# Performance work log

Measured on AMD Instinct MI355X. Metric: run time of the kernel, lower is better.

## Reference

```python
import jax, jax.numpy as jnp
import numpy as np

ALPHA = 0.01  # LeakyReLU negative slope


def setup_inputs() -> dict:
    key = jax.random.key(0)
    k1, k2, k3 = jax.random.split(key, 3)
    B, T, F, U, E = 32, 512, 128, 64, 32
    x = jax.random.normal(k1, (B, T, F), dtype=jnp.float32)
    Wg = jax.random.normal(k2, (F, E), dtype=jnp.float32) * (1.0 / np.sqrt(F))
    bg = jnp.zeros((E,), dtype=jnp.float32)
    We = jax.random.normal(k3, (E, F, U), dtype=jnp.float32) * (1.0 / np.sqrt(F))
    be = jnp.zeros((E, U), dtype=jnp.float32)
    return {"x": x, "Wg": Wg, "bg": bg, "We": We, "be": be}


def reference(x, Wg, bg, We, be):
    # gate: linear (no softmax in the original)
    gate = jnp.einsum('btf,fe->bte', x, Wg) + bg            # [B,T,E]
    # all experts as one batched GEMM: [B,T,U,E]
    h = jnp.einsum('btf,efu->btue', x, We) + be.T            # be.T: [U,E]
    h = jnp.where(h >= 0, h, ALPHA * h)                      # LeakyReLU
    # weighted sum over experts
    out = jnp.einsum('btue,bte->btu', h, gate)               # [B,T,U]
    return out
```

## Files before the change

### kernel.cpp

```cpp
#include <hip/hip_runtime.h>
#include <stdint.h>

#define N_TOK 16384
#define F_DIM 128
#define U_DIM 64
#define E_DIM 32

typedef __bf16 bf16x8 __attribute__((ext_vector_type(8)));
typedef float  floatx4 __attribute__((ext_vector_type(4)));

#define MFMA16(a, b, c) __builtin_amdgcn_mfma_f32_16x16x32_bf16((a), (b), (c), 0, 0, 0)

__device__ __forceinline__ unsigned short f2bf(float f) {
  union { float f; unsigned u; } v; v.f = f;
  unsigned r = v.u + 0x7FFFu + ((v.u >> 16) & 1u);
  return (unsigned short)(r >> 16);
}

__global__ __launch_bounds__(512, 1) void moe_main(
    const float* __restrict__ x,
    const float* __restrict__ Wg,
    const float* __restrict__ bg,
    const float* __restrict__ We,
    const float* __restrict__ be,
    float* __restrict__ out) {
  __shared__ unsigned short Xs[64 * 136];
  __shared__ float Gs[E_DIM][68];

  const int tid  = threadIdx.x;
  const int lane = tid & 63;
  const int wid  = tid >> 6;
  const int quad = lane >> 4;
  const int l15  = lane & 15;
  const int wr   = wid >> 2;
  const int wc   = wid & 3;
  const int u    = wc * 16 + l15;
  const int base = blockIdx.x * 64;

  float bw[4][4][8];
  float bevb[4];
  {
    const float* wsrc = We + (size_t)(quad * 8) * 64 + u;
#pragma unroll
    for (int e0 = 0; e0 < 3; e0++) {
#pragma unroll
      for (int ks = 0; ks < 4; ks++)
#pragma unroll
        for (int j = 0; j < 8; j++)
          bw[e0][ks][j] = wsrc[(size_t)e0 * 8192 + (ks * 32 + j) * 64];
      bevb[e0] = be[e0 * U_DIM + u];
    }
  }

  {
    const int row = tid >> 3;
    const int c16 = tid & 7;
    const float4* src = (const float4*)(x + (size_t)(base + row) * F_DIM + c16 * 16);
    float4 v0 = src[0], v1 = src[1], v2 = src[2], v3 = src[3];
    union { unsigned short us[16]; uint4 q[2]; } pk;
    pk.us[0]  = f2bf(v0.x); pk.us[1]  = f2bf(v0.y); pk.us[2]  = f2bf(v0.z); pk.us[3]  = f2bf(v0.w);
    pk.us[4]  = f2bf(v1.x); pk.us[5]  = f2bf(v1.y); pk.us[6]  = f2bf(v1.z); pk.us[7]  = f2bf(v1.w);
    pk.us[8]  = f2bf(v2.x); pk.us[9]  = f2bf(v2.y); pk.us[10] = f2bf(v2.z); pk.us[11] = f2bf(v2.w);
    pk.us[12] = f2bf(v3.x); pk.us[13] = f2bf(v3.y); pk.us[14] = f2bf(v3.z); pk.us[15] = f2bf(v3.w);
    uint4* dst = (uint4*)&Xs[row * 136 + c16 * 16];
    dst[0] = pk.q[0];
    dst[1] = pk.q[1];
  }
  __syncthreads();

  {
    const int rg = wid >> 1;
    const int et = wid & 1;
    bf16x8 ag[4];
#pragma unroll
    for (int ks = 0; ks < 4; ks++)
      ag[ks] = *(const bf16x8*)&Xs[(rg * 16 + l15) * 136 + ks * 32 + quad * 8];
    floatx4 g = {0.f, 0.f, 0.f, 0.f};
#pragma unroll
    for (int ks = 0; ks < 4; ks++) {
      union { unsigned short us[8]; bf16x8 v; } p;
#pragma unroll
      for (int j = 0; j < 8; j++)
        p.us[j] = f2bf(Wg[(size_t)(ks * 32 + quad * 8 + j) * 32 + et * 16 + l15]);
      g = MFMA16(ag[ks], p.v, g);
    }
    float bgv = bg[et * 16 + l15];
#pragma unroll
    for (int r = 0; r < 4; r++)
      Gs[et * 16 + l15][rg * 16 + quad * 4 + r] = g[r] + bgv;
  }

  bf16x8 a[2][4];
#pragma unroll
  for (int mb = 0; mb < 2; mb++)
#pragma unroll
    for (int ks = 0; ks < 4; ks++)
      a[mb][ks] = *(const bf16x8*)&Xs[(wr * 32 + mb * 16 + l15) * 136 + ks * 32 + quad * 8];
  __syncthreads();

  float oacc[8];
#pragma unroll
  for (int i = 0; i < 8; i++) oacc[i] = 0.f;

  float4 gbuf[2][2];
#pragma unroll
  for (int mb = 0; mb < 2; mb++)
    gbuf[0][mb] = *(const float4*)&Gs[0][wr * 32 + mb * 16 + quad * 4];

  const float* wbase = We + (size_t)(quad * 8) * 64 + u;

#pragma unroll 4
  for (int e = 0; e < E_DIM; ++e) {
    const int c = e & 3;
    const int gp = e & 1;

    if (e + 3 < E_DIM) {
#pragma unroll
      for (int ks = 0; ks < 4; ks++)
#pragma unroll
        for (int j = 0; j < 8; j++)
          bw[(e + 3) & 3][ks][j] = wbase[(size_t)(e + 3) * 8192 + (ks * 32 + j) * 64];
      bevb[(e + 3) & 3] = be[(e + 3) * U_DIM + u];
    }
    if (e + 1 < E_DIM) {
#pragma unroll
      for (int mb = 0; mb < 2; mb++)
        gbuf[gp ^ 1][mb] = *(const float4*)&Gs[e + 1][wr * 32 + mb * 16 + quad * 4];
    }

    bf16x8 bb[4];
#pragma unroll
    for (int ks = 0; ks < 4; ks++) {
      union { unsigned short us[8]; bf16x8 v; } p;
#pragma unroll
      for (int j = 0; j < 8; j++) p.us[j] = f2bf(bw[c][ks][j]);
      bb[ks] = p.v;
    }

    const float bev = bevb[c];
    floatx4 h[2];
#pragma unroll
    for (int mb = 0; mb < 2; mb++) h[mb] = {bev, bev, bev, bev};
#pragma unroll
    for (int ks = 0; ks < 4; ks++)
#pragma unroll
      for (int mb = 0; mb < 2; mb++)
        h[mb] = MFMA16(a[mb][ks], bb[ks], h[mb]);

#pragma unroll
    for (int mb = 0; mb < 2; mb++) {
      const float4 g4 = gbuf[gp][mb];
      const float gr[4] = {g4.x, g4.y, g4.z, g4.w};
#pragma unroll
      for (int r = 0; r < 4; r++) {
        float t = h[mb][r];
        t = fmaxf(t, 0.01f * t);
        oacc[mb * 4 + r] = fmaf(gr[r], t, oacc[mb * 4 + r]);
      }
    }
  }

#pragma unroll
  for (int mb = 0; mb < 2; mb++)
#pragma unroll
    for (int r = 0; r < 4; r++)
      out[(size_t)(base + wr * 32 + mb * 16 + quad * 4 + r) * U_DIM + u] = oacc[mb * 4 + r];
}

extern "C" void kernel_launch(void* const* d_in, const int* in_sizes, int n_in,
                              void* d_out, int out_size, void* d_ws, size_t ws_size,
                              hipStream_t stream) {
  const float* x  = (const float*)d_in[0];
  const float* Wg = (const float*)d_in[1];
  const float* bg = (const float*)d_in[2];
  const float* We = (const float*)d_in[3];
  const float* be = (const float*)d_in[4];
  (void)in_sizes; (void)n_in; (void)out_size; (void)d_ws; (void)ws_size;

  moe_main<<<N_TOK / 64, 512, 0, stream>>>(x, Wg, bg, We, be, (float*)d_out);
}
```

Baseline: 97.54 us.

## Stage expert weights cooperatively through double-buffered LDS as bf16

Previously every wave loaded its own fp32 copy of each expert's weight slice from global memory and converted it to bf16 itself, which is redundant because waves sharing columns load the same data. Now the 512 threads cooperatively load each expert's 128x64 weight matrix once per block, convert it to bf16, and store it into a double-buffered LDS array. The MFMA loop reads B fragments from LDS and waits on a barrier each expert iteration. This cuts global traffic and per-wave conversion work, but adds a barrier per expert and extra LDS use and traffic.

```diff
diff --git a/kernel.cpp b/kernel.cpp
--- a/kernel.cpp
+++ b/kernel.cpp
@@ -17,15 +17,23 @@
   return (unsigned short)(r >> 16);
 }
 
-__global__ __launch_bounds__(512, 1) void moe_main(
+__device__ __forceinline__ uint4 cvt8pack(const float* w) {
+  union { __bf16 b[8]; uint4 q; } p;
+#pragma unroll
+  for (int j = 0; j < 8; j++) p.b[j] = (__bf16)w[j];
+  return p.q;
+}
+
+__global__ __launch_bounds__(512, 1) void moe_fused(
     const float* __restrict__ x,
     const float* __restrict__ Wg,
     const float* __restrict__ bg,
     const float* __restrict__ We,
     const float* __restrict__ be,
     float* __restrict__ out) {
-  __shared__ unsigned short Xs[64 * 136];
-  __shared__ float Gs[E_DIM][68];
+  __shared__ __align__(16) unsigned short Xs[64 * 136];
+  __shared__ __align__(16) float Gs[E_DIM][68];
+  __shared__ __align__(16) unsigned short Bs[2][16 * 528];
 
   const int tid  = threadIdx.x;
   const int lane = tid & 63;
@@ -37,20 +45,14 @@
   const int u    = wc * 16 + l15;
   const int base = blockIdx.x * 64;
 
-  float bw[4][4][8];
-  float bevb[4];
-  {
-    const float* wsrc = We + (size_t)(quad * 8) * 64 + u;
+  const int f0 = (wid >> 2) * 32 + (wid & 3) * 8;
+  const float* ws0 = We + f0 * 64 + lane;
+
+  float w0[8], w1[8];
 #pragma unroll
-    for (int e0 = 0; e0 < 3; e0++) {
-#pragma unroll
-      for (int ks = 0; ks < 4; ks++)
-#pragma unroll
-        for (int j = 0; j < 8; j++)
-          bw[e0][ks][j] = wsrc[(size_t)e0 * 8192 + (ks * 32 + j) * 64];
-      bevb[e0] = be[e0 * U_DIM + u];
-    }
-  }
+  for (int j = 0; j < 8; j++) { w0[j] = ws0[j * 64]; w1[j] = ws0[4096 + j * 64]; }
+  float bevCur = be[u];
+  float bevNxt = be[U_DIM + u];
 
   {
     const int row = tid >> 3;
@@ -66,6 +68,11 @@
     dst[0] = pk.q[0];
     dst[1] = pk.q[1];
   }
+
+  *(uint4*)&Bs[0][wid * 528 + lane * 8]       = cvt8pack(w0);
+  *(uint4*)&Bs[0][(wid + 8) * 528 + lane * 8] = cvt8pack(w1);
+#pragma unroll
+  for (int j = 0; j < 8; j++) { w0[j] = ws0[8192 + j * 64]; w1[j] = ws0[8192 + 4096 + j * 64]; }
   __syncthreads();
 
   {
@@ -102,61 +109,56 @@
 #pragma unroll
   for (int i = 0; i < 8; i++) oacc[i] = 0.f;
 
-  float4 gbuf[2][2];
+  const unsigned short* rB = Bs[0];
+  unsigned short*       wB = Bs[1];
+
+  for (int e = 0; e < E_DIM; ++e) {
+    bf16x8 bb[4];
 #pragma unroll
-  for (int mb = 0; mb < 2; mb++)
-    gbuf[0][mb] = *(const float4*)&Gs[0][wr * 32 + mb * 16 + quad * 4];
+    for (int ks = 0; ks < 4; ks++)
+      bb[ks] = *(const bf16x8*)&rB[(ks * 4 + quad) * 528 + u * 8];
+    float4 gc0 = *(const float4*)&Gs[e][wr * 32 + quad * 4];
+    float4 gc1 = *(const float4*)&Gs[e][wr * 32 + 16 + quad * 4];
 
-  const float* wbase = We + (size_t)(quad * 8) * 64 + u;
+    if (e < E_DIM - 1) {
+      *(uint4*)&wB[wid * 528 + lane * 8]       = cvt8pack(w0);
+      *(uint4*)&wB[(wid + 8) * 528 + lane * 8] = cvt8pack(w1);
+      if (e < E_DIM - 2) {
+        const float* s = ws0 + (size_t)(e + 2) * 8192;
+#pragma unroll
+        for (int j = 0; j < 8; j++) { w0[j] = s[j * 64]; w1[j] = s[4096 + j * 64]; }
+      }
+    }
+    float bevNew = (e < E_DIM - 2) ? be[(e + 2) * U_DIM + u] : 0.f;
 
-#pragma unroll 4
-  for (int e = 0; e < E_DIM; ++e) {
-    const int c = e & 3;
-    const int gp = e & 1;
+    asm volatile("s_waitcnt lgkmcnt(0)" ::: "memory");
+    __builtin_amdgcn_sched_barrier(0);
 
-    if (e + 3 < E_DIM) {
+    floatx4 h0 = {bevCur, bevCur, bevCur, bevCur};
+    floatx4 h1 = h0;
 #pragma unroll
-      for (int ks = 0; ks < 4; ks++)
-#pragma unroll
-        for (int j = 0; j < 8; j++)
-          bw[(e + 3) & 3][ks][j] = wbase[(size_t)(e + 3) * 8192 + (ks * 32 + j) * 64];
-      bevb[(e + 3) & 3] = be[(e + 3) * U_DIM + u];
-    }
-    if (e + 1 < E_DIM) {
-#pragma unroll
-      for (int mb = 0; mb < 2; mb++)
-        gbuf[gp ^ 1][mb] = *(const float4*)&Gs[e + 1][wr * 32 + mb * 16 + quad * 4];
+    for (int ks = 0; ks < 4; ks++) {
+      h0 = MFMA16(a[0][ks], bb[ks], h0);
+      h1 = MFMA16(a[1][ks], bb[ks], h1);
     }
 
-    bf16x8 bb[4];
-#pragma unroll
-    for (int ks = 0; ks < 4; ks++) {
-      union { unsigned short us[8]; bf16x8 v; } p;
-#pragma unroll
-      for (int j = 0; j < 8; j++) p.us[j] = f2bf(bw[c][ks][j]);
-      bb[ks] = p.v;
-    }
-
-    const float bev = bevb[c];
-    floatx4 h[2];
-#pragma unroll
-    for (int mb = 0; mb < 2; mb++) h[mb] = {bev, bev, bev, bev};
-#pragma unroll
-    for (int ks = 0; ks < 4; ks++)
-#pragma unroll
-      for (int mb = 0; mb < 2; mb++)
-        h[mb] = MFMA16(a[mb][ks], bb[ks], h[mb]);
-
-#pragma unroll
-    for (int mb = 0; mb < 2; mb++) {
-      const float4 g4 = gbuf[gp][mb];
-      const float gr[4] = {g4.x, g4.y, g4.z, g4.w};
+    {
+      const float g0[4] = {gc0.x, gc0.y, gc0.z, gc0.w};
+      const float g1[4] = {gc1.x, gc1.y, gc1.z, gc1.w};
 #pragma unroll
       for (int r = 0; r < 4; r++) {
-        float t = h[mb][r];
-        t = fmaxf(t, 0.01f * t);
-        oacc[mb * 4 + r] = fmaf(gr[r], t, oacc[mb * 4 + r]);
+        float t0 = h0[r]; t0 = fmaxf(t0, 0.01f * t0);
+        oacc[r]     = fmaf(g0[r], t0, oacc[r]);
+        float t1 = h1[r]; t1 = fmaxf(t1, 0.01f * t1);
+        oacc[4 + r] = fmaf(g1[r], t1, oacc[4 + r]);
       }
+    }
+    bevCur = bevNxt;
+    bevNxt = bevNew;
+
+    if (e < E_DIM - 1) {
+      __builtin_amdgcn_s_barrier();
+      const unsigned short* t = rB; rB = wB; wB = (unsigned short*)t;
     }
   }
 
@@ -177,5 +179,5 @@
   const float* be = (const float*)d_in[4];
   (void)in_sizes; (void)n_in; (void)out_size; (void)d_ws; (void)ws_size;
 
-  moe_main<<<N_TOK / 64, 512, 0, stream>>>(x, Wg, bg, We, be, (float*)d_out);
+  moe_fused<<<N_TOK / 64, 512, 0, stream>>>(x, Wg, bg, We, be, (float*)d_out);
 }
```

After: 87.47 us. -10.3%, faster.
